# Kernel tuning notes

Hardware: AMD Instinct MI355X
Metric: run time of the kernel (lower is better)

## Reference

```python
import jax, jax.numpy as jnp
import numpy as np

NUM_USERS = 50000
NUM_ITEMS = 100000
N_NODES = NUM_USERS + NUM_ITEMS
NNZ = 2400000
EMBED = 64
N_LAYERS = 3
BATCH = 4096
NEG_SLOPE = 0.2
EPS = 1e-12


def setup_inputs() -> dict:
    key = jax.random.key(0)
    ks = jax.random.split(key, 12)
    return {
        "edge_val": jax.random.uniform(ks[0], (NNZ,), jnp.float32) * 0.01,
        "embed_user": jax.random.normal(ks[1], (NUM_USERS, EMBED), jnp.float32) * 0.1,
        "embed_item": jax.random.normal(ks[2], (NUM_ITEMS, EMBED), jnp.float32) * 0.1,
        "W1_w": jax.random.normal(ks[3], (N_LAYERS, EMBED, EMBED), jnp.float32) * 0.2,
        "W1_b": jnp.zeros((N_LAYERS, EMBED), jnp.float32),
        "W2_w": jax.random.normal(ks[4], (N_LAYERS, EMBED, EMBED), jnp.float32) * 0.2,
        "W2_b": jnp.zeros((N_LAYERS, EMBED), jnp.float32),
        "edge_row": jax.random.randint(ks[5], (NNZ,), 0, N_NODES, jnp.int32),
        "edge_col": jax.random.randint(ks[6], (NNZ,), 0, N_NODES, jnp.int32),
        "batch_user": jax.random.randint(ks[7], (BATCH,), 0, NUM_USERS, jnp.int32),
        "batch_pos_item": jax.random.randint(ks[8], (BATCH,), 0, NUM_ITEMS, jnp.int32),
        "batch_neg_item": jax.random.randint(ks[9], (BATCH,), 0, NUM_ITEMS, jnp.int32),
    }


def _ngcf_embeddings(edge_val, embed_user, embed_item, W1_w, W1_b, W2_w, W2_b,
                     edge_row, edge_col):
    E = jnp.concatenate([embed_user, embed_item], axis=0)  # [N, d]
    embs = [E]
    for i in range(N_LAYERS):
        # SpMM: (L @ E)[r] = sum over edges e with row r of val[e] * E[col[e]]
        msgs = edge_val[:, None] * E[edge_col]  # [nnz, d]
        LE = jax.ops.segment_sum(msgs, edge_row, num_segments=N_NODES)
        # I is identity -> (L + I) @ E = LE + E
        ego = (LE + E) @ W1_w[i].T + W1_b[i]
        side = LE @ W2_w[i].T + W2_b[i]
        E = jax.nn.leaky_relu(ego + side, negative_slope=NEG_SLOPE)
        # message dropout p=0 is identity; L2-normalize per node (F.normalize)
        norm = jnp.linalg.norm(E, axis=1, keepdims=True)
        E = E / jnp.maximum(norm, EPS)
        embs.append(E)
    return jnp.concatenate(embs, axis=1)  # [N, (1+L)*d]


def reference(edge_val, embed_user, embed_item, W1_w, W1_b, W2_w, W2_b,
              edge_row, edge_col, batch_user, batch_pos_item, batch_neg_item):
    G = _ngcf_embeddings(edge_val, embed_user, embed_item, W1_w, W1_b, W2_w,
                         W2_b, edge_row, edge_col)
    user_g = G[:NUM_USERS]
    item_g = G[NUM_USERS:]
    return (user_g[batch_user], item_g[batch_pos_item], item_g[batch_neg_item])
```

## Files before the change

### kernel.cpp

```cpp
#include <hip/hip_runtime.h>
#include <hip/hip_fp16.h>

#define NUM_USERS 50000
#define NUM_ITEMS 100000
#define N_NODES   150000
#define EMBED     64
#define BATCH     4096
#define NNZ       2400000
#define NB        586
#define CBITS     10
#define NCOARSE   147
#define CAP       20480
#define TILE      4096
#define NTILES    9375

typedef _Float16 half8 __attribute__((ext_vector_type(8)));
typedef float    f32x4 __attribute__((ext_vector_type(4)));

__device__ __forceinline__ float bf2f(unsigned short u) {
    union { unsigned int u32; float f; } v; v.u32 = ((unsigned int)u) << 16; return v.f;
}
__device__ __forceinline__ float getf(const void* p, int i, int fbf) {
    if (fbf) return bf2f(((const unsigned short*)p)[i]);
    return ((const float*)p)[i];
}
__device__ __forceinline__ int geti(const void* p, int i, int i64) {
    if (i64) return (int)(((const long long*)p)[i]);
    return ((const int*)p)[i];
}
__device__ __forceinline__ int clampi(int v, int lo, int hi) {
    return v < lo ? lo : (v > hi ? hi : v);
}
__device__ __forceinline__ float h2f(unsigned short u) {
    return __half2float(__ushort_as_half(u));
}
__device__ __forceinline__ unsigned short f2h(float f) {
    return __half_as_ushort(__float2half(f));
}

__global__ void k_flags_r22(const unsigned short* __restrict__ ev,
                            const void* __restrict__ er, int* __restrict__ fl) {
    if (threadIdx.x == 0 && blockIdx.x == 0) {
        int good = 0;
        for (int i = 0; i < 64; ++i) {
            float f = bf2f(ev[i]);
            if (f >= 0.0f && f <= 0.011f) good++;
        }
        fl[0] = (good >= 60) ? 1 : 0;
        int ok = 0;
        for (int i = 0; i < 64; ++i) {
            long long v = ((const long long*)er)[i];
            if (v >= 0 && v < (long long)N_NODES) ok++;
        }
        fl[1] = (ok >= 60) ? 1 : 0;
    }
}

__global__ void k_probe_r22(int* __restrict__ fl) {
    __shared__ unsigned short A[16 * 32];
    __shared__ unsigned short B[32 * 16];
    const int lane = threadIdx.x;
    for (int i = lane; i < 512; i += 64) {
        int r = i >> 5, k = i & 31;
        A[i] = f2h(((r * 7 + k * 3) % 23) * 0.04f - 0.4f);
    }
    for (int i = lane; i < 512; i += 64) {
        int k = i >> 4, n = i & 15;
        B[i] = f2h(((k * 11 + n * 5) % 19) * 0.05f - 0.45f);
    }
    __syncthreads();
    union { unsigned short u[8]; half8 h; } ua, ub;
    const int rA = lane & 15;
    const int g  = lane >> 4;
    #pragma unroll
    for (int e = 0; e < 8; ++e) {
        ua.u[e] = A[rA * 32 + g * 8 + e];
        ub.u[e] = B[(g * 8 + e) * 16 + rA];
    }
    f32x4 acc = {0.f, 0.f, 0.f, 0.f};
    acc = __builtin_amdgcn_mfma_f32_16x16x32_f16(ua.h, ub.h, acc, 0, 0, 0);
    bool ok = true;
    #pragma unroll
    for (int reg = 0; reg < 4; ++reg) {
        int row = g * 4 + reg;
        int col = lane & 15;
        float ref = 0.0f;
        for (int k = 0; k < 32; ++k)
            ref += h2f(A[row * 32 + k]) * h2f(B[k * 16 + col]);
        if (fabsf(acc[reg] - ref) > 0.02f * fmaxf(1.0f, fabsf(ref))) ok = false;
    }
    unsigned long long m = __ballot(ok);
    if (lane == 0) fl[2] = (m == ~0ull) ? 1 : 0;
}

__global__ void k_init_r22(const void* __restrict__ eu, const void* __restrict__ ei,
                           const int* __restrict__ fl, unsigned short* __restrict__ Eh) {
    int fbf = fl[0];
    int i = blockIdx.x * 256 + threadIdx.x;
    if (i < N_NODES * EMBED) {
        int r = i >> 6;
        float v;
        if (r < NUM_USERS) v = getf(eu, i, fbf);
        else               v = getf(ei, i - NUM_USERS * EMBED, fbf);
        Eh[i] = f2h(v);
    }
}

__global__ __launch_bounds__(256) void k_partA_r22(const void* __restrict__ ev,
                                                   const void* __restrict__ er,
                                                   const void* __restrict__ ec,
                                                   const int* __restrict__ fl,
                                                   int* __restrict__ ccur,
                                                   int2* __restrict__ tmp) {
    __shared__ int2 stage[TILE];
    __shared__ int  hist[NCOARSE];
    __shared__ int  base[NCOARSE];
    const int t   = threadIdx.x;
    const int i64 = fl[1], fbf = fl[0];
    for (int i = t; i < NCOARSE; i += 256) hist[i] = 0;
    __syncthreads();

    int  bx[16], ps[16];
    int2 pk[16];
    const int t0 = blockIdx.x * TILE;
    #pragma unroll
    for (int k = 0; k < 16; ++k) {
        int e = t0 + k * 256 + t;
        bx[k] = -1;
        if (e < NNZ) {
            int r = clampi(geti(er, e, i64), 0, N_NODES - 1);
            int c = clampi(geti(ec, e, i64), 0, N_NODES - 1);
            float v = getf(ev, e, fbf);
            int b = r >> CBITS;
            bx[k] = b;
            pk[k] = make_int2(((r & 1023) << 18) | c, __float_as_int(v));
            ps[k] = atomicAdd(&hist[b], 1);
        }
    }
    __syncthreads();
    if (t == 0) {
        int run = 0;
        for (int i = 0; i < NCOARSE; ++i) { base[i] = run; run += hist[i]; }
    }
    __syncthreads();
    #pragma unroll
    for (int k = 0; k < 16; ++k)
        if (bx[k] >= 0) stage[base[bx[k]] + ps[k]] = pk[k];
    __syncthreads();

    for (int b = t; b < NCOARSE; b += 256) {
        int n = hist[b];
        if (n == 0) continue;
        int g = atomicAdd(&ccur[b], n);
        int2* dst = tmp + (size_t)b * CAP;
        int s0 = base[b];
        for (int i = 0; i < n && (g + i) < CAP; ++i) dst[g + i] = stage[s0 + i];
    }
}

__global__ __launch_bounds__(256) void k_histB1_r22(const int* __restrict__ ccur,
                                                    const int2* __restrict__ tmp,
                                                    int* __restrict__ cnt) {
    __shared__ int h[1024];
    const int b = blockIdx.x;
    const int t = threadIdx.x;
    const int base_row = b << CBITS;
    int nrow = N_NODES - base_row; if (nrow > 1024) nrow = 1024;
    for (int i = t; i < 1024; i += 256) h[i] = 0;
    __syncthreads();
    int n = ccur[b]; if (n > CAP) n = CAP;
    const int2* src = tmp + (size_t)b * CAP;
    for (int p = t; p < n; p += 256) {
        int rl = src[p].x >> 18;
        atomicAdd(&h[rl], 1);
    }
    __syncthreads();
    for (int i = t; i < nrow; i += 256) cnt[base_row + i] = h[i];
}

__global__ __launch_bounds__(256) void k_scanA_r22(const int* __restrict__ cnt,
                                                   int* __restrict__ bsum) {
    int i = blockIdx.x * 256 + threadIdx.x;
    int v = (i < N_NODES) ? cnt[i] : 0;
    #pragma unroll
    for (int d = 1; d < 64; d <<= 1) v += __shfl_xor(v, d, 64);
    __shared__ int sh[4];
    if ((threadIdx.x & 63) == 0) sh[threadIdx.x >> 6] = v;
    __syncthreads();
    if (threadIdx.x == 0) bsum[blockIdx.x] = sh[0] + sh[1] + sh[2] + sh[3];
}

__global__ __launch_bounds__(1024) void k_scanB_r22(int* __restrict__ bsum) {
    __shared__ int sh[1024];
    int t = threadIdx.x;
    if (t < NB) sh[t] = bsum[t];
    __syncthreads();
    if (t == 0) {
        int run = 0;
        for (int i = 0; i < NB; ++i) { int x = sh[i]; sh[i] = run; run += x; }
    }
    __syncthreads();
    if (t < NB) bsum[t] = sh[t];
}

__global__ __launch_bounds__(256) void k_scanC_r22(const int* __restrict__ cnt,
                                                   const int* __restrict__ bsum,
                                                   int* __restrict__ rowptr) {
    __shared__ int sh[256];
    int i = blockIdx.x * 256 + threadIdx.x;
    int t = threadIdx.x;
    sh[t] = (i < N_NODES) ? cnt[i] : 0;
    __syncthreads();
    if (t == 0) {
        int run = bsum[blockIdx.x];
        for (int k = 0; k < 256; ++k) { int x = sh[k]; sh[k] = run; run += x; }
    }
    __syncthreads();
    if (i < N_NODES) rowptr[i] = sh[t];
    if (i == 0) rowptr[N_NODES] = NNZ;
}

__global__ __launch_bounds__(256) void k_place_r22(const int* __restrict__ ccur,
                                                   const int2* __restrict__ tmp,
                                                   const int* __restrict__ rowptr,
                                                   int2* __restrict__ colcv) {
    __shared__ int rp[1025];
    __shared__ int cur[1024];
    const int b = blockIdx.x;
    const int t = threadIdx.x;
    const int base_row = b << CBITS;
    int nrow = N_NODES - base_row; if (nrow > 1024) nrow = 1024;
    for (int i = t; i <= nrow; i += 256) rp[i] = rowptr[base_row + i];
    for (int i = t; i < 1024; i += 256) cur[i] = 0;
    __syncthreads();
    int n = ccur[b]; if (n > CAP) n = CAP;
    const int2* src = tmp + (size_t)b * CAP;
    for (int p = t; p < n; p += 256) {
        int2 cv = src[p];
        int rl = cv.x >> 18;
        int c  = cv.x & 0x3FFFF;
        int dst = rp[rl] + atomicAdd(&cur[rl], 1);
        colcv[dst] = make_int2(c, cv.y);
    }
}

__global__ __launch_bounds__(256) void k_gath_r22(const int* __restrict__ rowptr,
                                                  const int2* __restrict__ colcv,
                                                  const unsigned short* __restrict__ Eh,
                                                  unsigned short* __restrict__ LEh) {
    int r = blockIdx.x * 4 + (threadIdx.x >> 6);
    if (r >= N_NODES) return;
    const int lane = threadIdx.x & 63;
    const int g = lane >> 4;
    const int q = lane & 15;
    const int s = rowptr[r];
    const int e = rowptr[r + 1];

    float a0 = 0.f, a1 = 0.f, a2 = 0.f, a3 = 0.f;

    for (int base = s; base < e; base += 64) {
        int idx = base + lane;
        int2 cv = make_int2(0, 0);
        if (idx < e) cv = colcv[idx];
        int m = e - base; if (m > 64) m = 64;

        for (int j = 0; j < m; j += 8) {
            int i0 = j + g;
            int i1 = j + 4 + g;
            bool v0 = i0 < m;
            bool v1 = i1 < m;
            int   c0 = __shfl(cv.x, i0, 64);
            float f0 = __int_as_float(__shfl(cv.y, i0, 64));
            int   c1 = __shfl(cv.x, i1, 64);
            float f1 = __int_as_float(__shfl(cv.y, i1, 64));
            c0 = v0 ? c0 : 0;  f0 = v0 ? f0 : 0.0f;
            c1 = v1 ? c1 : 0;  f1 = v1 ? f1 : 0.0f;
            ushort4 p0 = *reinterpret_cast<const ushort4*>(&Eh[c0 * EMBED + 4 * q]);
            ushort4 p1 = *reinterpret_cast<const ushort4*>(&Eh[c1 * EMBED + 4 * q]);
            a0 = fmaf(f0, h2f(p0.x), a0);
            a1 = fmaf(f0, h2f(p0.y), a1);
            a2 = fmaf(f0, h2f(p0.z), a2);
            a3 = fmaf(f0, h2f(p0.w), a3);
            a0 = fmaf(f1, h2f(p1.x), a0);
            a1 = fmaf(f1, h2f(p1.y), a1);
            a2 = fmaf(f1, h2f(p1.z), a2);
            a3 = fmaf(f1, h2f(p1.w), a3);
        }
    }

    #pragma unroll
    for (int d = 16; d < 64; d <<= 1) {
        a0 += __shfl_xor(a0, d, 64);
        a1 += __shfl_xor(a1, d, 64);
        a2 += __shfl_xor(a2, d, 64);
        a3 += __shfl_xor(a3, d, 64);
    }
    if (g == 0) {
        ushort4 o;
        o.x = f2h(a0); o.y = f2h(a1); o.z = f2h(a2); o.w = f2h(a3);
        *reinterpret_cast<ushort4*>(&LEh[r * EMBED + 4 * q]) = o;
    }
}

__global__ __launch_bounds__(256) void k_mlp_r22(unsigned short* __restrict__ Eh,
                                                 const unsigned short* __restrict__ LEh,
                                                 const void* __restrict__ W1,
                                                 const void* __restrict__ B1,
                                                 const void* __restrict__ W2,
                                                 const void* __restrict__ B2,
                                                 const int* __restrict__ fl, int layer) {
    __shared__ unsigned short W12s[64 * 72];
    __shared__ unsigned short W1s [64 * 72];
    __shared__ float4 XA[4][16];
    __shared__ float4 XB[4][16];
    const int fbf  = fl[0];
    const int mfok = fl[2];
    const int wofs = layer * EMBED * EMBED;
    const int bofs = layer * EMBED;
    const int t    = threadIdx.x;
    const int lane = t & 63;
    const int w    = t >> 6;

    if (mfok) {
        for (int i = t; i < 4096; i += 256) {
            int n = i >> 6, k = i & 63;
            float w1 = getf(W1, wofs + i, fbf);
            float w2 = getf(W2, wofs + i, fbf);
            W1s [n * 72 + k] = f2h(w1);
            W12s[n * 72 + k] = f2h(w1 + w2);
        }
        __syncthreads();

        const int cl = lane & 15;
        const int g  = lane >> 4;

        float bias[4];
        #pragma unroll
        for (int nt = 0; nt < 4; ++nt)
            bias[nt] = getf(B1, bofs + nt * 16 + cl, fbf) + getf(B2, bofs + nt * 16 + cl, fbf);

        half8 bw12_0[4], bw12_1[4], bw1_0[4], bw1_1[4];
        #pragma unroll
        for (int nt = 0; nt < 4; ++nt) {
            const int nrow = (nt * 16 + cl) * 72;
            bw12_0[nt] = *reinterpret_cast<const half8*>(&W12s[nrow + 0  + g * 8]);
            bw12_1[nt] = *reinterpret_cast<const half8*>(&W12s[nrow + 32 + g * 8]);
            bw1_0 [nt] = *reinterpret_cast<const half8*>(&W1s [nrow + 0  + g * 8]);
            bw1_1 [nt] = *reinterpret_cast<const half8*>(&W1s [nrow + 32 + g * 8]);
        }

        const int gw = blockIdx.x * 4 + w;
        const int nw = gridDim.x * 4;

        for (int tile = gw; tile < NTILES; tile += nw) {
            const int r0 = tile * 16;
            const unsigned short* lerow = &LEh[(r0 + cl) * EMBED];
            const unsigned short* erow  = &Eh [(r0 + cl) * EMBED];
            half8 aLE0 = *reinterpret_cast<const half8*>(&lerow[0  + g * 8]);
            half8 aLE1 = *reinterpret_cast<const half8*>(&lerow[32 + g * 8]);
            half8 aE0  = *reinterpret_cast<const half8*>(&erow [0  + g * 8]);
            half8 aE1  = *reinterpret_cast<const half8*>(&erow [32 + g * 8]);

            f32x4 acc0 = {bias[0], bias[0], bias[0], bias[0]};
            f32x4 acc1 = {bias[1], bias[1], bias[1], bias[1]};
            f32x4 acc2 = {bias[2], bias[2], bias[2], bias[2]};
            f32x4 acc3 = {bias[3], bias[3], bias[3], bias[3]};

            acc0 = __builtin_amdgcn_mfma_f32_16x16x32_f16(aLE0, bw12_0[0], acc0, 0, 0, 0);
            acc1 = __builtin_amdgcn_mfma_f32_16x16x32_f16(aLE0, bw12_0[1], acc1, 0, 0, 0);
            acc2 = __builtin_amdgcn_mfma_f32_16x16x32_f16(aLE0, bw12_0[2], acc2, 0, 0, 0);
            acc3 = __builtin_amdgcn_mfma_f32_16x16x32_f16(aLE0, bw12_0[3], acc3, 0, 0, 0);
            acc0 = __builtin_amdgcn_mfma_f32_16x16x32_f16(aLE1, bw12_1[0], acc0, 0, 0, 0);
            acc1 = __builtin_amdgcn_mfma_f32_16x16x32_f16(aLE1, bw12_1[1], acc1, 0, 0, 0);
            acc2 = __builtin_amdgcn_mfma_f32_16x16x32_f16(aLE1, bw12_1[2], acc2, 0, 0, 0);
            acc3 = __builtin_amdgcn_mfma_f32_16x16x32_f16(aLE1, bw12_1[3], acc3, 0, 0, 0);
            acc0 = __builtin_amdgcn_mfma_f32_16x16x32_f16(aE0,  bw1_0 [0], acc0, 0, 0, 0);
            acc1 = __builtin_amdgcn_mfma_f32_16x16x32_f16(aE0,  bw1_0 [1], acc1, 0, 0, 0);
            acc2 = __builtin_amdgcn_mfma_f32_16x16x32_f16(aE0,  bw1_0 [2], acc2, 0, 0, 0);
            acc3 = __builtin_amdgcn_mfma_f32_16x16x32_f16(aE0,  bw1_0 [3], acc3, 0, 0, 0);
            acc0 = __builtin_amdgcn_mfma_f32_16x16x32_f16(aE1,  bw1_1 [0], acc0, 0, 0, 0);
            acc1 = __builtin_amdgcn_mfma_f32_16x16x32_f16(aE1,  bw1_1 [1], acc1, 0, 0, 0);
            acc2 = __builtin_amdgcn_mfma_f32_16x16x32_f16(aE1,  bw1_1 [2], acc2, 0, 0, 0);
            acc3 = __builtin_amdgcn_mfma_f32_16x16x32_f16(aE1,  bw1_1 [3], acc3, 0, 0, 0);

            f32x4 h0, h1, h2, h3;
            float p0 = 0.f, p1 = 0.f, p2 = 0.f, p3 = 0.f;
            #pragma unroll
            for (int rg = 0; rg < 4; ++rg) {
                float a = acc0[rg]; float hh = (a > 0.f) ? a : 0.2f * a; h0[rg] = hh;
                float s = hh * hh;
                a = acc1[rg]; hh = (a > 0.f) ? a : 0.2f * a; h1[rg] = hh; s += hh * hh;
                a = acc2[rg]; hh = (a > 0.f) ? a : 0.2f * a; h2[rg] = hh; s += hh * hh;
                a = acc3[rg]; hh = (a > 0.f) ? a : 0.2f * a; h3[rg] = hh; s += hh * hh;
                if (rg == 0) p0 = s; else if (rg == 1) p1 = s; else if (rg == 2) p2 = s; else p3 = s;
            }
            #pragma unroll
            for (int d = 1; d < 16; d <<= 1) {
                p0 += __shfl_xor(p0, d, 64);
                p1 += __shfl_xor(p1, d, 64);
                p2 += __shfl_xor(p2, d, 64);
                p3 += __shfl_xor(p3, d, 64);
            }
            float inv0 = 1.0f / fmaxf(sqrtf(p0), 1e-12f);
            float inv1 = 1.0f / fmaxf(sqrtf(p1), 1e-12f);
            float inv2 = 1.0f / fmaxf(sqrtf(p2), 1e-12f);
            float inv3 = 1.0f / fmaxf(sqrtf(p3), 1e-12f);

            #pragma unroll
            for (int rg = 0; rg < 4; ++rg) {
                float inv = (rg == 0) ? inv0 : (rg == 1) ? inv1 : (rg == 2) ? inv2 : inv3;
                unsigned short* orow = &Eh[(r0 + g * 4 + rg) * EMBED + cl];
                orow[0]  = f2h(h0[rg] * inv);
                orow[16] = f2h(h1[rg] * inv);
                orow[32] = f2h(h2[rg] * inv);
                orow[48] = f2h(h3[rg] * inv);
            }
        }
        return;
    }

    float w1r[64], w12r[64];
    if (fbf) {
        const unsigned short* p1 = (const unsigned short*)W1 + wofs + lane * 64;
        const unsigned short* p2 = (const unsigned short*)W2 + wofs + lane * 64;
        #pragma unroll
        for (int q = 0; q < 16; ++q) {
            ushort4 a = reinterpret_cast<const ushort4*>(p1)[q];
            ushort4 b = reinterpret_cast<const ushort4*>(p2)[q];
            float f0 = bf2f(a.x), f1 = bf2f(a.y), f2 = bf2f(a.z), f3 = bf2f(a.w);
            w1r[4*q+0] = f0; w1r[4*q+1] = f1; w1r[4*q+2] = f2; w1r[4*q+3] = f3;
            w12r[4*q+0] = f0 + bf2f(b.x); w12r[4*q+1] = f1 + bf2f(b.y);
            w12r[4*q+2] = f2 + bf2f(b.z); w12r[4*q+3] = f3 + bf2f(b.w);
        }
    } else {
        const float* p1 = (const float*)W1 + wofs + lane * 64;
        const float* p2 = (const float*)W2 + wofs + lane * 64;
        #pragma unroll
        for (int q = 0; q < 16; ++q) {
            float4 a = reinterpret_cast<const float4*>(p1)[q];
            float4 b = reinterpret_cast<const float4*>(p2)[q];
            w1r[4*q+0] = a.x; w1r[4*q+1] = a.y; w1r[4*q+2] = a.z; w1r[4*q+3] = a.w;
            w12r[4*q+0] = a.x + b.x; w12r[4*q+1] = a.y + b.y;
            w12r[4*q+2] = a.z + b.z; w12r[4*q+3] = a.w + b.w;
        }
    }
    const float bias = getf(B1, bofs + lane, fbf) + getf(B2, bofs + lane, fbf);

    const int gw = blockIdx.x * 4 + w;
    const int nw = gridDim.x * 4;

    int row = gw;
    float le = 0.0f, ee = 0.0f;
    if (row < N_NODES) {
        le = h2f(LEh[row * EMBED + lane]);
        ee = h2f(Eh[row * EMBED + lane]);
    }
    while (row < N_NODES) {
        const int nrow = row + nw;
        float nle = 0.0f, nee = 0.0f;
        if (nrow < N_NODES) {
            nle = h2f(LEh[nrow * EMBED + lane]);
            nee = h2f(Eh[nrow * EMBED + lane]);
        }

        ((float*)&XA[w][0])[lane] = le;
        ((float*)&XB[w][0])[lane] = ee;
        float acc0 = bias, acc1 = 0.0f;
        #pragma unroll
        for (int q = 0; q < 16; ++q) {
            float4 a = XA[w][q];
            float4 b = XB[w][q];
            acc0 = fmaf(a.x, w12r[4*q+0], acc0);
            acc1 = fmaf(b.x, w1r [4*q+0], acc1);
            acc0 = fmaf(a.y, w12r[4*q+1], acc0);
            acc1 = fmaf(b.y, w1r [4*q+1], acc1);
            acc0 = fmaf(a.z, w12r[4*q+2], acc0);
            acc1 = fmaf(b.z, w1r [4*q+2], acc1);
            acc0 = fmaf(a.w, w12r[4*q+3], acc0);
            acc1 = fmaf(b.w, w1r [4*q+3], acc1);
        }
        float acc = acc0 + acc1;
        float h = (acc > 0.0f) ? acc : 0.2f * acc;

        float s = h * h;
        #pragma unroll
        for (int d = 1; d < 64; d <<= 1) s += __shfl_xor(s, d, 64);
        const float inv = 1.0f / fmaxf(sqrtf(s), 1e-12f);

        Eh[row * EMBED + lane] = f2h(h * inv);

        row = nrow; le = nle; ee = nee;
    }
}

__global__ void k_pick_r22(const unsigned short* __restrict__ Eh, const void* __restrict__ bu,
                           const void* __restrict__ bp, const void* __restrict__ bn,
                           const int* __restrict__ fl,
                           float* __restrict__ out, int stage) {
    int i64 = fl[1];
    int i = blockIdx.x * 256 + threadIdx.x;
    if (i >= 3 * BATCH * EMBED) return;
    int c = i & 63;
    int row = i >> 6;
    int o = row >> 12;
    int b = row & 4095;
    int idx;
    if (o == 0)      idx = geti(bu, b, i64);
    else if (o == 1) idx = geti(bp, b, i64);
    else             idx = geti(bn, b, i64);
    int src;
    if (o == 0) src = clampi(idx, 0, NUM_USERS - 1);
    else        src = NUM_USERS + clampi(idx, 0, NUM_ITEMS - 1);
    int pos = o * (BATCH * 256) + b * 256 + stage * 64 + c;
    out[pos] = h2f(Eh[src * EMBED + c]);
}

extern "C" void kernel_launch(void* const* d_in, const int* in_sizes, int n_in,
                              void* d_out, int out_size, void* d_ws, size_t ws_size,
                              hipStream_t stream) {
    const void* edge_val = d_in[0];
    const void* emb_u    = d_in[1];
    const void* emb_i    = d_in[2];
    const void* W1w      = d_in[3];
    const void* W1b      = d_in[4];
    const void* W2w      = d_in[5];
    const void* W2b      = d_in[6];
    const void* erow     = d_in[7];
    const void* ecol     = d_in[8];
    const void* bu       = d_in[9];
    const void* bp       = d_in[10];
    const void* bn       = d_in[11];

    const size_t EHB  = (size_t)N_NODES * EMBED * 2;
    const size_t RPB  = 600064;
    const size_t CNB  = 600064;
    const size_t BSB  = 4096;
    const size_t CCB  = 4096;
    const size_t CVB2 = (size_t)NNZ * sizeof(int2);
    const size_t TMPB = (size_t)NCOARSE * CAP * sizeof(int2);

    const size_t need = 256 + 2 * EHB + RPB + CNB + BSB + CCB + CVB2 + TMPB;
    if (ws_size < need) return;

    char* ws = (char*)d_ws;
    int*            fl     = (int*)ws;
    unsigned short* Eh     = (unsigned short*)(ws + 256);
    unsigned short* LEh    = (unsigned short*)(ws + 256 + EHB);
    int*            rowptr = (int*)(ws + 256 + 2 * EHB);
    int*            cnt    = (int*)(ws + 256 + 2 * EHB + RPB);
    int*            bsum   = (int*)(ws + 256 + 2 * EHB + RPB + CNB);
    int*            ccur   = (int*)(ws + 256 + 2 * EHB + RPB + CNB + BSB);
    int2*           colcv  = (int2*)(ws + 256 + 2 * EHB + RPB + CNB + BSB + CCB);
    int2*           tmpcv  = (int2*)(ws + 256 + 2 * EHB + RPB + CNB + BSB + CCB + CVB2);
    float*          out    = (float*)d_out;

    k_flags_r22<<<1, 64, 0, stream>>>((const unsigned short*)edge_val, erow, fl);
    k_probe_r22<<<1, 64, 0, stream>>>(fl);

    k_init_r22<<<(N_NODES * EMBED + 255) / 256, 256, 0, stream>>>(emb_u, emb_i, fl, Eh);

    hipMemsetAsync(ccur, 0, CCB, stream);
    k_partA_r22<<<(NNZ + TILE - 1) / TILE, 256, 0, stream>>>(edge_val, erow, ecol, fl,
                                                             ccur, tmpcv);
    k_histB1_r22<<<NCOARSE, 256, 0, stream>>>(ccur, tmpcv, cnt);
    k_scanA_r22<<<NB, 256, 0, stream>>>(cnt, bsum);
    k_scanB_r22<<<1, 1024, 0, stream>>>(bsum);
    k_scanC_r22<<<NB, 256, 0, stream>>>(cnt, bsum, rowptr);
    k_place_r22<<<NCOARSE, 256, 0, stream>>>(ccur, tmpcv, rowptr, colcv);

    k_pick_r22<<<(3 * BATCH * EMBED + 255) / 256, 256, 0, stream>>>(Eh, bu, bp, bn, fl, out, 0);

    for (int l = 0; l < 3; ++l) {
        k_gath_r22<<<(N_NODES + 3) / 4, 256, 0, stream>>>(rowptr, colcv, Eh, LEh);
        k_mlp_r22<<<2048, 256, 0, stream>>>(Eh, LEh, W1w, W1b, W2w, W2b, fl, l);
        k_pick_r22<<<(3 * BATCH * EMBED + 255) / 256, 256, 0, stream>>>(Eh, bu, bp, bn, fl, out, l + 1);
    }
}
```

Measured before the change: 518.4 us.

## Fuse SpMM gather with MFMA MLP per 16-row tile, ping-pong embedding buffers

```diff
diff --git a/kernel.cpp b/kernel.cpp
--- a/kernel.cpp
+++ b/kernel.cpp
@@ -38,7 +38,7 @@
     return __half_as_ushort(__float2half(f));
 }
 
-__global__ void k_flags_r22(const unsigned short* __restrict__ ev,
+__global__ void k_flags_r23(const unsigned short* __restrict__ ev,
                             const void* __restrict__ er, int* __restrict__ fl) {
     if (threadIdx.x == 0 && blockIdx.x == 0) {
         int good = 0;
@@ -56,7 +56,7 @@
     }
 }
 
-__global__ void k_probe_r22(int* __restrict__ fl) {
+__global__ void k_probe_r23(int* __restrict__ fl) {
     __shared__ unsigned short A[16 * 32];
     __shared__ unsigned short B[32 * 16];
     const int lane = threadIdx.x;
@@ -93,7 +93,7 @@
     if (lane == 0) fl[2] = (m == ~0ull) ? 1 : 0;
 }
 
-__global__ void k_init_r22(const void* __restrict__ eu, const void* __restrict__ ei,
+__global__ void k_init_r23(const void* __restrict__ eu, const void* __restrict__ ei,
                            const int* __restrict__ fl, unsigned short* __restrict__ Eh) {
     int fbf = fl[0];
     int i = blockIdx.x * 256 + threadIdx.x;
@@ -106,7 +106,7 @@
     }
 }
 
-__global__ __launch_bounds__(256) void k_partA_r22(const void* __restrict__ ev,
+__global__ __launch_bounds__(256) void k_partA_r23(const void* __restrict__ ev,
                                                    const void* __restrict__ er,
                                                    const void* __restrict__ ec,
                                                    const int* __restrict__ fl,
@@ -158,7 +158,7 @@
     }
 }
 
-__global__ __launch_bounds__(256) void k_histB1_r22(const int* __restrict__ ccur,
+__global__ __launch_bounds__(256) void k_histB1_r23(const int* __restrict__ ccur,
                                                     const int2* __restrict__ tmp,
                                                     int* __restrict__ cnt) {
     __shared__ int h[1024];
@@ -178,7 +178,7 @@
     for (int i = t; i < nrow; i += 256) cnt[base_row + i] = h[i];
 }
 
-__global__ __launch_bounds__(256) void k_scanA_r22(const int* __restrict__ cnt,
+__global__ __launch_bounds__(256) void k_scanA_r23(const int* __restrict__ cnt,
                                                    int* __restrict__ bsum) {
     int i = blockIdx.x * 256 + threadIdx.x;
     int v = (i < N_NODES) ? cnt[i] : 0;
@@ -190,7 +190,7 @@
     if (threadIdx.x == 0) bsum[blockIdx.x] = sh[0] + sh[1] + sh[2] + sh[3];
 }
 
-__global__ __launch_bounds__(1024) void k_scanB_r22(int* __restrict__ bsum) {
+__global__ __launch_bounds__(1024) void k_scanB_r23(int* __restrict__ bsum) {
     __shared__ int sh[1024];
     int t = threadIdx.x;
     if (t < NB) sh[t] = bsum[t];
@@ -203,7 +203,7 @@
     if (t < NB) bsum[t] = sh[t];
 }
 
-__global__ __launch_bounds__(256) void k_scanC_r22(const int* __restrict__ cnt,
+__global__ __launch_bounds__(256) void k_scanC_r23(const int* __restrict__ cnt,
                                                    const int* __restrict__ bsum,
                                                    int* __restrict__ rowptr) {
     __shared__ int sh[256];
@@ -220,7 +220,7 @@
     if (i == 0) rowptr[N_NODES] = NNZ;
 }
 
-__global__ __launch_bounds__(256) void k_place_r22(const int* __restrict__ ccur,
+__global__ __launch_bounds__(256) void k_place_r23(const int* __restrict__ ccur,
                                                    const int2* __restrict__ tmp,
                                                    const int* __restrict__ rowptr,
                                                    int2* __restrict__ colcv) {
@@ -244,75 +244,19 @@
     }
 }
 
-__global__ __launch_bounds__(256) void k_gath_r22(const int* __restrict__ rowptr,
+__global__ __launch_bounds__(256) void k_fuse_r23(const int* __restrict__ rowptr,
                                                   const int2* __restrict__ colcv,
-                                                  const unsigned short* __restrict__ Eh,
-                                                  unsigned short* __restrict__ LEh) {
-    int r = blockIdx.x * 4 + (threadIdx.x >> 6);
-    if (r >= N_NODES) return;
-    const int lane = threadIdx.x & 63;
-    const int g = lane >> 4;
-    const int q = lane & 15;
-    const int s = rowptr[r];
-    const int e = rowptr[r + 1];
-
-    float a0 = 0.f, a1 = 0.f, a2 = 0.f, a3 = 0.f;
-
-    for (int base = s; base < e; base += 64) {
-        int idx = base + lane;
-        int2 cv = make_int2(0, 0);
-        if (idx < e) cv = colcv[idx];
-        int m = e - base; if (m > 64) m = 64;
-
-        for (int j = 0; j < m; j += 8) {
-            int i0 = j + g;
-            int i1 = j + 4 + g;
-            bool v0 = i0 < m;
-            bool v1 = i1 < m;
-            int   c0 = __shfl(cv.x, i0, 64);
-            float f0 = __int_as_float(__shfl(cv.y, i0, 64));
-            int   c1 = __shfl(cv.x, i1, 64);
-            float f1 = __int_as_float(__shfl(cv.y, i1, 64));
-            c0 = v0 ? c0 : 0;  f0 = v0 ? f0 : 0.0f;
-            c1 = v1 ? c1 : 0;  f1 = v1 ? f1 : 0.0f;
-            ushort4 p0 = *reinterpret_cast<const ushort4*>(&Eh[c0 * EMBED + 4 * q]);
-            ushort4 p1 = *reinterpret_cast<const ushort4*>(&Eh[c1 * EMBED + 4 * q]);
-            a0 = fmaf(f0, h2f(p0.x), a0);
-            a1 = fmaf(f0, h2f(p0.y), a1);
-            a2 = fmaf(f0, h2f(p0.z), a2);
-            a3 = fmaf(f0, h2f(p0.w), a3);
-            a0 = fmaf(f1, h2f(p1.x), a0);
-            a1 = fmaf(f1, h2f(p1.y), a1);
-            a2 = fmaf(f1, h2f(p1.z), a2);
-            a3 = fmaf(f1, h2f(p1.w), a3);
-        }
-    }
-
-    #pragma unroll
-    for (int d = 16; d < 64; d <<= 1) {
-        a0 += __shfl_xor(a0, d, 64);
-        a1 += __shfl_xor(a1, d, 64);
-        a2 += __shfl_xor(a2, d, 64);
-        a3 += __shfl_xor(a3, d, 64);
-    }
-    if (g == 0) {
-        ushort4 o;
-        o.x = f2h(a0); o.y = f2h(a1); o.z = f2h(a2); o.w = f2h(a3);
-        *reinterpret_cast<ushort4*>(&LEh[r * EMBED + 4 * q]) = o;
-    }
-}
-
-__global__ __launch_bounds__(256) void k_mlp_r22(unsigned short* __restrict__ Eh,
-                                                 const unsigned short* __restrict__ LEh,
-                                                 const void* __restrict__ W1,
-                                                 const void* __restrict__ B1,
-                                                 const void* __restrict__ W2,
-                                                 const void* __restrict__ B2,
-                                                 const int* __restrict__ fl, int layer) {
+                                                  const unsigned short* __restrict__ Ein,
+                                                  unsigned short* __restrict__ Eout,
+                                                  unsigned short* __restrict__ LEh,
+                                                  const void* __restrict__ W1,
+                                                  const void* __restrict__ B1,
+                                                  const void* __restrict__ W2,
+                                                  const void* __restrict__ B2,
+                                                  const int* __restrict__ fl, int layer) {
     __shared__ unsigned short W12s[64 * 72];
     __shared__ unsigned short W1s [64 * 72];
-    __shared__ float4 XA[4][16];
-    __shared__ float4 XB[4][16];
+    __shared__ unsigned short LEt[4][16 * 72];
     const int fbf  = fl[0];
     const int mfok = fl[2];
     const int wofs = layer * EMBED * EMBED;
@@ -320,104 +264,160 @@
     const int t    = threadIdx.x;
     const int lane = t & 63;
     const int w    = t >> 6;
+    const int g    = lane >> 4;
+    const int q    = lane & 15;
 
     if (mfok) {
         for (int i = t; i < 4096; i += 256) {
-            int n = i >> 6, k = i & 63;
+            int idx = (i >> 6) * 72 + (i & 63);
             float w1 = getf(W1, wofs + i, fbf);
             float w2 = getf(W2, wofs + i, fbf);
-            W1s [n * 72 + k] = f2h(w1);
-            W12s[n * 72 + k] = f2h(w1 + w2);
+            W1s [idx] = f2h(w1);
+            W12s[idx] = f2h(w1 + w2);
         }
         __syncthreads();
-
-        const int cl = lane & 15;
-        const int g  = lane >> 4;
-
-        float bias[4];
-        #pragma unroll
-        for (int nt = 0; nt < 4; ++nt)
-            bias[nt] = getf(B1, bofs + nt * 16 + cl, fbf) + getf(B2, bofs + nt * 16 + cl, fbf);
-
-        half8 bw12_0[4], bw12_1[4], bw1_0[4], bw1_1[4];
-        #pragma unroll
-        for (int nt = 0; nt < 4; ++nt) {
-            const int nrow = (nt * 16 + cl) * 72;
-            bw12_0[nt] = *reinterpret_cast<const half8*>(&W12s[nrow + 0  + g * 8]);
-            bw12_1[nt] = *reinterpret_cast<const half8*>(&W12s[nrow + 32 + g * 8]);
-            bw1_0 [nt] = *reinterpret_cast<const half8*>(&W1s [nrow + 0  + g * 8]);
-            bw1_1 [nt] = *reinterpret_cast<const half8*>(&W1s [nrow + 32 + g * 8]);
-        }
-
-        const int gw = blockIdx.x * 4 + w;
-        const int nw = gridDim.x * 4;
-
-        for (int tile = gw; tile < NTILES; tile += nw) {
-            const int r0 = tile * 16;
-            const unsigned short* lerow = &LEh[(r0 + cl) * EMBED];
-            const unsigned short* erow  = &Eh [(r0 + cl) * EMBED];
-            half8 aLE0 = *reinterpret_cast<const half8*>(&lerow[0  + g * 8]);
-            half8 aLE1 = *reinterpret_cast<const half8*>(&lerow[32 + g * 8]);
-            half8 aE0  = *reinterpret_cast<const half8*>(&erow [0  + g * 8]);
-            half8 aE1  = *reinterpret_cast<const half8*>(&erow [32 + g * 8]);
-
-            f32x4 acc0 = {bias[0], bias[0], bias[0], bias[0]};
-            f32x4 acc1 = {bias[1], bias[1], bias[1], bias[1]};
-            f32x4 acc2 = {bias[2], bias[2], bias[2], bias[2]};
-            f32x4 acc3 = {bias[3], bias[3], bias[3], bias[3]};
-
-            acc0 = __builtin_amdgcn_mfma_f32_16x16x32_f16(aLE0, bw12_0[0], acc0, 0, 0, 0);
-            acc1 = __builtin_amdgcn_mfma_f32_16x16x32_f16(aLE0, bw12_0[1], acc1, 0, 0, 0);
-            acc2 = __builtin_amdgcn_mfma_f32_16x16x32_f16(aLE0, bw12_0[2], acc2, 0, 0, 0);
-            acc3 = __builtin_amdgcn_mfma_f32_16x16x32_f16(aLE0, bw12_0[3], acc3, 0, 0, 0);
-            acc0 = __builtin_amdgcn_mfma_f32_16x16x32_f16(aLE1, bw12_1[0], acc0, 0, 0, 0);
-            acc1 = __builtin_amdgcn_mfma_f32_16x16x32_f16(aLE1, bw12_1[1], acc1, 0, 0, 0);
-            acc2 = __builtin_amdgcn_mfma_f32_16x16x32_f16(aLE1, bw12_1[2], acc2, 0, 0, 0);
-            acc3 = __builtin_amdgcn_mfma_f32_16x16x32_f16(aLE1, bw12_1[3], acc3, 0, 0, 0);
-            acc0 = __builtin_amdgcn_mfma_f32_16x16x32_f16(aE0,  bw1_0 [0], acc0, 0, 0, 0);
-            acc1 = __builtin_amdgcn_mfma_f32_16x16x32_f16(aE0,  bw1_0 [1], acc1, 0, 0, 0);
-            acc2 = __builtin_amdgcn_mfma_f32_16x16x32_f16(aE0,  bw1_0 [2], acc2, 0, 0, 0);
-            acc3 = __builtin_amdgcn_mfma_f32_16x16x32_f16(aE0,  bw1_0 [3], acc3, 0, 0, 0);
-            acc0 = __builtin_amdgcn_mfma_f32_16x16x32_f16(aE1,  bw1_1 [0], acc0, 0, 0, 0);
-            acc1 = __builtin_amdgcn_mfma_f32_16x16x32_f16(aE1,  bw1_1 [1], acc1, 0, 0, 0);
-            acc2 = __builtin_amdgcn_mfma_f32_16x16x32_f16(aE1,  bw1_1 [2], acc2, 0, 0, 0);
-            acc3 = __builtin_amdgcn_mfma_f32_16x16x32_f16(aE1,  bw1_1 [3], acc3, 0, 0, 0);
-
-            f32x4 h0, h1, h2, h3;
-            float p0 = 0.f, p1 = 0.f, p2 = 0.f, p3 = 0.f;
-            #pragma unroll
-            for (int rg = 0; rg < 4; ++rg) {
-                float a = acc0[rg]; float hh = (a > 0.f) ? a : 0.2f * a; h0[rg] = hh;
-                float s = hh * hh;
-                a = acc1[rg]; hh = (a > 0.f) ? a : 0.2f * a; h1[rg] = hh; s += hh * hh;
-                a = acc2[rg]; hh = (a > 0.f) ? a : 0.2f * a; h2[rg] = hh; s += hh * hh;
-                a = acc3[rg]; hh = (a > 0.f) ? a : 0.2f * a; h3[rg] = hh; s += hh * hh;
-                if (rg == 0) p0 = s; else if (rg == 1) p1 = s; else if (rg == 2) p2 = s; else p3 = s;
+    }
+
+    float bias[4];
+    #pragma unroll
+    for (int nt = 0; nt < 4; ++nt)
+        bias[nt] = getf(B1, bofs + nt * 16 + q, fbf) + getf(B2, bofs + nt * 16 + q, fbf);
+
+    const int gw = blockIdx.x * 4 + w;
+    const int nw = gridDim.x * 4;
+
+    for (int tile = gw; tile < NTILES; tile += nw) {
+        const int r0 = tile * 16;
+
+        for (int rr = 0; rr < 16; ++rr) {
+            const int row = r0 + rr;
+            const int s = rowptr[row];
+            const int e = rowptr[row + 1];
+            float a0 = 0.f, a1 = 0.f, a2 = 0.f, a3 = 0.f;
+            for (int base = s; base < e; base += 64) {
+                int idx = base + lane;
+                int2 cv = make_int2(0, 0);
+                if (idx < e) cv = colcv[idx];
+                int m = e - base; if (m > 64) m = 64;
+                for (int j = 0; j < m; j += 8) {
+                    int i0 = j + g;
+                    int i1 = j + 4 + g;
+                    bool v0 = i0 < m;
+                    bool v1 = i1 < m;
+                    int   c0 = __shfl(cv.x, i0, 64);
+                    float f0 = __int_as_float(__shfl(cv.y, i0, 64));
+                    int   c1 = __shfl(cv.x, i1, 64);
+                    float f1 = __int_as_float(__shfl(cv.y, i1, 64));
+                    c0 = v0 ? c0 : 0;  f0 = v0 ? f0 : 0.0f;
+                    c1 = v1 ? c1 : 0;  f1 = v1 ? f1 : 0.0f;
+                    ushort4 p0 = *reinterpret_cast<const ushort4*>(&Ein[c0 * EMBED + 4 * q]);
+                    ushort4 p1 = *reinterpret_cast<const ushort4*>(&Ein[c1 * EMBED + 4 * q]);
+                    a0 = fmaf(f0, h2f(p0.x), a0);
+                    a1 = fmaf(f0, h2f(p0.y), a1);
+                    a2 = fmaf(f0, h2f(p0.z), a2);
+                    a3 = fmaf(f0, h2f(p0.w), a3);
+                    a0 = fmaf(f1, h2f(p1.x), a0);
+                    a1 = fmaf(f1, h2f(p1.y), a1);
+                    a2 = fmaf(f1, h2f(p1.z), a2);
+                    a3 = fmaf(f1, h2f(p1.w), a3);
+                }
             }
             #pragma unroll
-            for (int d = 1; d < 16; d <<= 1) {
-                p0 += __shfl_xor(p0, d, 64);
-                p1 += __shfl_xor(p1, d, 64);
-                p2 += __shfl_xor(p2, d, 64);
-                p3 += __shfl_xor(p3, d, 64);
+            for (int d = 16; d < 64; d <<= 1) {
+                a0 += __shfl_xor(a0, d, 64);
+                a1 += __shfl_xor(a1, d, 64);
+                a2 += __shfl_xor(a2, d, 64);
+                a3 += __shfl_xor(a3, d, 64);
             }
-            float inv0 = 1.0f / fmaxf(sqrtf(p0), 1e-12f);
-            float inv1 = 1.0f / fmaxf(sqrtf(p1), 1e-12f);
-            float inv2 = 1.0f / fmaxf(sqrtf(p2), 1e-12f);
-            float inv3 = 1.0f / fmaxf(sqrtf(p3), 1e-12f);
-
-            #pragma unroll
-            for (int rg = 0; rg < 4; ++rg) {
-                float inv = (rg == 0) ? inv0 : (rg == 1) ? inv1 : (rg == 2) ? inv2 : inv3;
-                unsigned short* orow = &Eh[(r0 + g * 4 + rg) * EMBED + cl];
-                orow[0]  = f2h(h0[rg] * inv);
-                orow[16] = f2h(h1[rg] * inv);
-                orow[32] = f2h(h2[rg] * inv);
-                orow[48] = f2h(h3[rg] * inv);
+            if (g == 0) {
+                ushort4 o;
+                o.x = f2h(a0); o.y = f2h(a1); o.z = f2h(a2); o.w = f2h(a3);
+                if (mfok) {
+                    *reinterpret_cast<ushort4*>(&LEt[w][rr * 72 + 4 * q]) = o;
+                } else {
+                    *reinterpret_cast<ushort4*>(&LEh[row * EMBED + 4 * q]) = o;
+                }
             }
         }
-        return;
-    }
+        if (!mfok) continue;
+
+        half8 aLE0 = *reinterpret_cast<const half8*>(&LEt[w][q * 72 + 0  + g * 8]);
+        half8 aLE1 = *reinterpret_cast<const half8*>(&LEt[w][q * 72 + 32 + g * 8]);
+        const unsigned short* erow = &Ein[(r0 + q) * EMBED];
+        half8 aE0  = *reinterpret_cast<const half8*>(&erow[0  + g * 8]);
+        half8 aE1  = *reinterpret_cast<const half8*>(&erow[32 + g * 8]);
+
+        f32x4 acc0 = {bias[0], bias[0], bias[0], bias[0]};
+        f32x4 acc1 = {bias[1], bias[1], bias[1], bias[1]};
+        f32x4 acc2 = {bias[2], bias[2], bias[2], bias[2]};
+        f32x4 acc3 = {bias[3], bias[3], bias[3], bias[3]};
+
+        #pragma unroll
+        for (int nt = 0; nt < 4; ++nt) {
+            const int nrow = (nt * 16 + q) * 72;
+            half8 b12_0 = *reinterpret_cast<const half8*>(&W12s[nrow + 0  + g * 8]);
+            half8 b12_1 = *reinterpret_cast<const half8*>(&W12s[nrow + 32 + g * 8]);
+            half8 b1_0  = *reinterpret_cast<const half8*>(&W1s [nrow + 0  + g * 8]);
+            half8 b1_1  = *reinterpret_cast<const half8*>(&W1s [nrow + 32 + g * 8]);
+            f32x4 a = (nt == 0) ? acc0 : (nt == 1) ? acc1 : (nt == 2) ? acc2 : acc3;
+            a = __builtin_amdgcn_mfma_f32_16x16x32_f16(aLE0, b12_0, a, 0, 0, 0);
+            a = __builtin_amdgcn_mfma_f32_16x16x32_f16(aLE1, b12_1, a, 0, 0, 0);
+            a = __builtin_amdgcn_mfma_f32_16x16x32_f16(aE0,  b1_0,  a, 0, 0, 0);
+            a = __builtin_amdgcn_mfma_f32_16x16x32_f16(aE1,  b1_1,  a, 0, 0, 0);
+            if (nt == 0) acc0 = a; else if (nt == 1) acc1 = a; else if (nt == 2) acc2 = a; else acc3 = a;
+        }
+
+        f32x4 h0, h1, h2, h3;
+        float p0 = 0.f, p1 = 0.f, p2 = 0.f, p3 = 0.f;
+        #pragma unroll
+        for (int rg = 0; rg < 4; ++rg) {
+            float a = acc0[rg]; float hh = (a > 0.f) ? a : 0.2f * a; h0[rg] = hh;
+            float s = hh * hh;
+            a = acc1[rg]; hh = (a > 0.f) ? a : 0.2f * a; h1[rg] = hh; s += hh * hh;
+            a = acc2[rg]; hh = (a > 0.f) ? a : 0.2f * a; h2[rg] = hh; s += hh * hh;
+            a = acc3[rg]; hh = (a > 0.f) ? a : 0.2f * a; h3[rg] = hh; s += hh * hh;
+            if (rg == 0) p0 = s; else if (rg == 1) p1 = s; else if (rg == 2) p2 = s; else p3 = s;
+        }
+        #pragma unroll
+        for (int d = 1; d < 16; d <<= 1) {
+            p0 += __shfl_xor(p0, d, 64);
+            p1 += __shfl_xor(p1, d, 64);
+            p2 += __shfl_xor(p2, d, 64);
+            p3 += __shfl_xor(p3, d, 64);
+        }
+        float inv0 = 1.0f / fmaxf(sqrtf(p0), 1e-12f);
+        float inv1 = 1.0f / fmaxf(sqrtf(p1), 1e-12f);
+        float inv2 = 1.0f / fmaxf(sqrtf(p2), 1e-12f);
+        float inv3 = 1.0f / fmaxf(sqrtf(p3), 1e-12f);
+
+        #pragma unroll
+        for (int rg = 0; rg < 4; ++rg) {
+            float inv = (rg == 0) ? inv0 : (rg == 1) ? inv1 : (rg == 2) ? inv2 : inv3;
+            unsigned short* orow = &Eout[(r0 + g * 4 + rg) * EMBED + q];
+            orow[0]  = f2h(h0[rg] * inv);
+            orow[16] = f2h(h1[rg] * inv);
+            orow[32] = f2h(h2[rg] * inv);
+            orow[48] = f2h(h3[rg] * inv);
+        }
+    }
+}
+
+__global__ __launch_bounds__(256) void k_mlpfb_r23(const unsigned short* __restrict__ Ein,
+                                                   unsigned short* __restrict__ Eout,
+                                                   const unsigned short* __restrict__ LEh,
+                                                   const void* __restrict__ W1,
+                                                   const void* __restrict__ B1,
+                                                   const void* __restrict__ W2,
+                                                   const void* __restrict__ B2,
+                                                   const int* __restrict__ fl, int layer) {
+    if (fl[2]) return;
+    __shared__ float4 XA[4][16];
+    __shared__ float4 XB[4][16];
+    const int fbf  = fl[0];
+    const int wofs = layer * EMBED * EMBED;
+    const int bofs = layer * EMBED;
+    const int lane = threadIdx.x & 63;
+    const int w    = threadIdx.x >> 6;
 
     float w1r[64], w12r[64];
     if (fbf) {
@@ -448,21 +448,9 @@
 
     const int gw = blockIdx.x * 4 + w;
     const int nw = gridDim.x * 4;
-
-    int row = gw;
-    float le = 0.0f, ee = 0.0f;
-    if (row < N_NODES) {
-        le = h2f(LEh[row * EMBED + lane]);
-        ee = h2f(Eh[row * EMBED + lane]);
-    }
-    while (row < N_NODES) {
-        const int nrow = row + nw;
-        float nle = 0.0f, nee = 0.0f;
-        if (nrow < N_NODES) {
-            nle = h2f(LEh[nrow * EMBED + lane]);
-            nee = h2f(Eh[nrow * EMBED + lane]);
-        }
-
+    for (int row = gw; row < N_NODES; row += nw) {
+        float le = h2f(LEh[row * EMBED + lane]);
+        float ee = h2f(Ein[row * EMBED + lane]);
         ((float*)&XA[w][0])[lane] = le;
         ((float*)&XB[w][0])[lane] = ee;
         float acc0 = bias, acc1 = 0.0f;
@@ -481,19 +469,15 @@
         }
         float acc = acc0 + acc1;
         float h = (acc > 0.0f) ? acc : 0.2f * acc;
-
         float s = h * h;
         #pragma unroll
         for (int d = 1; d < 64; d <<= 1) s += __shfl_xor(s, d, 64);
         const float inv = 1.0f / fmaxf(sqrtf(s), 1e-12f);
-
-        Eh[row * EMBED + lane] = f2h(h * inv);
-
-        row = nrow; le = nle; ee = nee;
-    }
-}
-
-__global__ void k_pick_r22(const unsigned short* __restrict__ Eh, const void* __restrict__ bu,
+        Eout[row * EMBED + lane] = f2h(h * inv);
+    }
+}
+
+__global__ void k_pick_r23(const unsigned short* __restrict__ Eh, const void* __restrict__ bu,
                            const void* __restrict__ bp, const void* __restrict__ bn,
                            const int* __restrict__ fl,
                            float* __restrict__ out, int stage) {
@@ -544,35 +528,41 @@
 
     char* ws = (char*)d_ws;
     int*            fl     = (int*)ws;
-    unsigned short* Eh     = (unsigned short*)(ws + 256);
-    unsigned short* LEh    = (unsigned short*)(ws + 256 + EHB);
+    unsigned short* E0     = (unsigned short*)(ws + 256);
+    unsigned short* E1     = (unsigned short*)(ws + 256 + EHB);
     int*            rowptr = (int*)(ws + 256 + 2 * EHB);
     int*            cnt    = (int*)(ws + 256 + 2 * EHB + RPB);
     int*            bsum   = (int*)(ws + 256 + 2 * EHB + RPB + CNB);
     int*            ccur   = (int*)(ws + 256 + 2 * EHB + RPB + CNB + BSB);
     int2*           colcv  = (int2*)(ws + 256 + 2 * EHB + RPB + CNB + BSB + CCB);
     int2*           tmpcv  = (int2*)(ws + 256 + 2 * EHB + RPB + CNB + BSB + CCB + CVB2);
+    unsigned short* LEh    = (unsigned short*)tmpcv;
     float*          out    = (float*)d_out;
 
-    k_flags_r22<<<1, 64, 0, stream>>>((const unsigned short*)edge_val, erow, fl);
-    k_probe_r22<<<1, 64, 0, stream>>>(fl);
-
-    k_init_r22<<<(N_NODES * EMBED + 255) / 256, 256, 0, stream>>>(emb_u, emb_i, fl, Eh);
+    k_flags_r23<<<1, 64, 0, stream>>>((const unsigned short*)edge_val, erow, fl);
+    k_probe_r23<<<1, 64, 0, stream>>>(fl);
+
+    k_init_r23<<<(N_NODES * EMBED + 255) / 256, 256, 0, stream>>>(emb_u, emb_i, fl, E0);
 
     hipMemsetAsync(ccur, 0, CCB, stream);
-    k_partA_r22<<<(NNZ + TILE - 1) / TILE, 256, 0, stream>>>(edge_val, erow, ecol, fl,
+    k_partA_r23<<<(NNZ + TILE - 1) / TILE, 256, 0, stream>>>(edge_val, erow, ecol, fl,
                                                              ccur, tmpcv);
-    k_histB1_r22<<<NCOARSE, 256, 0, stream>>>(ccur, tmpcv, cnt);
-    k_scanA_r22<<<NB, 256, 0, stream>>>(cnt, bsum);
-    k_scanB_r22<<<1, 1024, 0, stream>>>(bsum);
-    k_scanC_r22<<<NB, 256, 0, stream>>>(cnt, bsum, rowptr);
-    k_place_r22<<<NCOARSE, 256, 0, stream>>>(ccur, tmpcv, rowptr, colcv);
-
-    k_pick_r22<<<(3 * BATCH * EMBED + 255) / 256, 256, 0, stream>>>(Eh, bu, bp, bn, fl, out, 0);
-
+    k_histB1_r23<<<NCOARSE, 256, 0, stream>>>(ccur, tmpcv, cnt);
+    k_scanA_r23<<<NB, 256, 0, stream>>>(cnt, bsum);
+    k_scanB_r23<<<1, 1024, 0, stream>>>(bsum);
+    k_scanC_r23<<<NB, 256, 0, stream>>>(cnt, bsum, rowptr);
+    k_place_r23<<<NCOARSE, 256, 0, stream>>>(ccur, tmpcv, rowptr, colcv);
+
+    k_pick_r23<<<(3 * BATCH * EMBED + 255) / 256, 256, 0, stream>>>(E0, bu, bp, bn, fl, out, 0);
+
+    unsigned short* Ecur = E0;
+    unsigned short* Enxt = E1;
     for (int l = 0; l < 3; ++l) {
-        k_gath_r22<<<(N_NODES + 3) / 4, 256, 0, stream>>>(rowptr, colcv, Eh, LEh);
-        k_mlp_r22<<<2048, 256, 0, stream>>>(Eh, LEh, W1w, W1b, W2w, W2b, fl, l);
-        k_pick_r22<<<(3 * BATCH * EMBED + 255) / 256, 256, 0, stream>>>(Eh, bu, bp, bn, fl, out, l + 1);
-    }
-}
+        k_fuse_r23<<<2048, 256, 0, stream>>>(rowptr, colcv, Ecur, Enxt, LEh,
+                                             W1w, W1b, W2w, W2b, fl, l);
+        k_mlpfb_r23<<<1280, 256, 0, stream>>>(Ecur, Enxt, LEh,
+                                              W1w, W1b, W2w, W2b, fl, l);
+        unsigned short* tmp = Ecur; Ecur = Enxt; Enxt = tmp;
+        k_pick_r23<<<(3 * BATCH * EMBED + 255) / 256, 256, 0, stream>>>(Ecur, bu, bp, bn, fl, out, l + 1);
+    }
+}
```

Result: no change. 526.3 us (+1.5%).
